# Kernel tuning notes

Measured on AMD Instinct MI355X. Metric: run time of the kernel, lower is better.

The kernel has to match this reference:

```python
import jax, jax.numpy as jnp
import numpy as np

D_MODEL = 1024
NUM_HEADS = 16
HEAD = D_MODEL // NUM_HEADS
SCALE = float(np.sqrt(D_MODEL))  # note: sqrt(d_model), as in source
LN_EPS = 1e-5


def setup_inputs() -> dict:
    key = jax.random.key(0)
    ks = jax.random.split(key, 12)
    B, Sq, Skv = 2, 2048, 2048
    s = 0.02
    return {
        "x": jax.random.normal(ks[0], (B, Sq, D_MODEL), jnp.float32),
        "enc_output": jax.random.normal(ks[1], (B, Skv, D_MODEL), jnp.float32),
        "Wq": jax.random.normal(ks[2], (D_MODEL, D_MODEL), jnp.float32) * s,
        "bq": jnp.zeros((D_MODEL,), jnp.float32),
        "Wk": jax.random.normal(ks[3], (D_MODEL, D_MODEL), jnp.float32) * s,
        "bk": jnp.zeros((D_MODEL,), jnp.float32),
        "Wv": jax.random.normal(ks[4], (D_MODEL, D_MODEL), jnp.float32) * s,
        "bv": jnp.zeros((D_MODEL,), jnp.float32),
        "Wo": jax.random.normal(ks[5], (D_MODEL, D_MODEL), jnp.float32) * s,
        "bo": jnp.zeros((D_MODEL,), jnp.float32),
        "gamma": jnp.ones((D_MODEL,), jnp.float32),
        "beta": jnp.zeros((D_MODEL,), jnp.float32),
    }


def _split_heads(t):
    B, S, _ = t.shape
    return t.reshape(B, S, NUM_HEADS, HEAD).transpose(0, 2, 1, 3)  # [B,H,S,hd]


def reference(x, enc_output, Wq, bq, Wk, bk, Wv, bv, Wo, bo, gamma, beta):
    q = _split_heads(x @ Wq.T + bq)           # [B,H,Sq,hd]
    k = _split_heads(enc_output @ Wk.T + bk)  # [B,H,Skv,hd]
    v = _split_heads(enc_output @ Wv.T + bv)  # [B,H,Skv,hd]
    scores = jnp.einsum("bhqd,bhkd->bhqk", q, k) / SCALE
    attn_weights = jax.nn.softmax(scores, axis=-1)  # dropout p=0 -> identity
    ctx = jnp.einsum("bhqk,bhkd->bhqd", attn_weights, v)
    B, H, Sq, hd = ctx.shape
    ctx = ctx.transpose(0, 2, 1, 3).reshape(B, Sq, H * hd)
    proj = ctx @ Wo.T + bo
    y = x + proj
    mu = jnp.mean(y, axis=-1, keepdims=True)
    var = jnp.var(y, axis=-1, keepdims=True)
    out = (y - mu) * jax.lax.rsqrt(var + LN_EPS) * gamma + beta
    return out, attn_weights
```

## Files before the change

### kernel.cpp

```cpp
#include <hip/hip_runtime.h>

typedef __attribute__((ext_vector_type(4))) float f32x4;
typedef __attribute__((ext_vector_type(8))) short bf16x8;
typedef __attribute__((ext_vector_type(4))) short s16x4;
typedef unsigned short u16;

#define GLOAD_LDS16(g, l)                                                      \
  __builtin_amdgcn_global_load_lds(                                            \
      (__attribute__((address_space(1))) const void*)(g),                      \
      (__attribute__((address_space(3))) void*)(l), 16, 0, 0)

static __device__ __forceinline__ u16 f2b(float f) {
  unsigned u = __builtin_bit_cast(unsigned, f);
  unsigned r = (u + 0x7fffu + ((u >> 16) & 1u)) >> 16;
  return (u16)r;
}

static __device__ __forceinline__ f32x4 mfma16(bf16x8 a, bf16x8 b, f32x4 c) {
  return __builtin_amdgcn_mfma_f32_16x16x32_bf16(a, b, c, 0, 0, 0);
}

static __device__ __forceinline__ int fsw(int row) {
  return (row & 7) ^ ((row & 8) >> 1);
}

__global__ __launch_bounds__(256) void cvt_bf16(const float* __restrict__ in,
                                                u16* __restrict__ out, int n4) {
  int i = blockIdx.x * 256 + threadIdx.x;
  int stride = gridDim.x * 256;
  for (; i < n4; i += stride) {
    float4 v = ((const float4*)in)[i];
    s16x4 o;
    o[0] = (short)f2b(v.x);
    o[1] = (short)f2b(v.y);
    o[2] = (short)f2b(v.z);
    o[3] = (short)f2b(v.w);
    ((s16x4*)out)[i] = o;
  }
}

#define QSCALE 0.0450842200278f
__global__ __launch_bounds__(256) void gemm_qkv3(
    const u16* __restrict__ xb, const u16* __restrict__ eb,
    const u16* __restrict__ Wqb, const u16* __restrict__ Wkb,
    const u16* __restrict__ Wvb, const float* __restrict__ bq,
    const float* __restrict__ bk, const float* __restrict__ bv,
    u16* __restrict__ Qd, u16* __restrict__ Kd, u16* __restrict__ Vtd) {
  __shared__ __align__(16) u16 As[128 * 32];
  __shared__ __align__(16) u16 Bs[128 * 32];
  const int K = 1024;
  int z = blockIdx.z;
  const u16* A = (z == 0) ? xb : eb;
  const u16* W = (z == 0) ? Wqb : (z == 1) ? Wkb : Wvb;
  const float* bias = (z == 0) ? bq : (z == 1) ? bk : bv;

  int tid = threadIdx.x;
  int w = tid >> 6, lane = tid & 63;
  int wr = w >> 1, wc = w & 1;
  int r16 = lane & 15, c4 = lane >> 4;
  int m0 = blockIdx.y * 128, n0 = blockIdx.x * 128;
  int srow = tid >> 2;
  int scol = (tid & 3) * 8;

  f32x4 acc[4][4] = {};

  const u16* ga0 = A + (size_t)(m0 + srow) * K + scol;
  const u16* gb0 = W + (size_t)(n0 + srow) * K + scol;
  char* asb = (char*)As + w * 1024;
  char* bsb = (char*)Bs + w * 1024;

  for (int k0 = 0; k0 < K; k0 += 32) {
    GLOAD_LDS16(ga0 + k0, asb);
    GLOAD_LDS16(ga0 + 64 * K + k0, asb + 4096);
    GLOAD_LDS16(gb0 + k0, bsb);
    GLOAD_LDS16(gb0 + 64 * K + k0, bsb + 4096);
    __syncthreads();
    bf16x8 af[4], bfr[4];
#pragma unroll
    for (int i = 0; i < 4; ++i)
      af[i] = *(const bf16x8*)(As + (wr * 64 + i * 16 + r16) * 32 + c4 * 8);
#pragma unroll
    for (int j = 0; j < 4; ++j)
      bfr[j] = *(const bf16x8*)(Bs + (wc * 64 + j * 16 + r16) * 32 + c4 * 8);
#pragma unroll
    for (int i = 0; i < 4; ++i)
#pragma unroll
      for (int j = 0; j < 4; ++j) acc[i][j] = mfma16(af[i], bfr[j], acc[i][j]);
    __syncthreads();
  }

  if (z < 2) {
    float oscale = (z == 0) ? QSCALE : 1.0f;
    u16* dst = (z == 0) ? Qd : Kd;
#pragma unroll
    for (int i = 0; i < 4; ++i) {
      int m = m0 + wr * 64 + i * 16 + c4 * 4;
      int b = m >> 11, s = m & 2047;
#pragma unroll
      for (int j = 0; j < 4; ++j) {
        int n = n0 + wc * 64 + j * 16 + r16;
        int h = n >> 6, d = n & 63;
        float bv = bias[n];
        u16* dp = dst + (((size_t)(b * 16 + h) * 2048 + s) * 64 + d);
#pragma unroll
        for (int r = 0; r < 4; ++r)
          dp[(size_t)r * 64] = f2b((acc[i][j][r] + bv) * oscale);
      }
    }
  } else {
#pragma unroll
    for (int i = 0; i < 4; ++i) {
      int m = m0 + wr * 64 + i * 16 + c4 * 4;
      int b = m >> 11, s = m & 2047;
#pragma unroll
      for (int j = 0; j < 4; ++j) {
        int n = n0 + wc * 64 + j * 16 + r16;
        int h = n >> 6, d = n & 63;
        float bv = bias[n];
        s16x4 o4;
#pragma unroll
        for (int r = 0; r < 4; ++r) o4[r] = (short)f2b(acc[i][j][r] + bv);
        *(s16x4*)(Vtd + ((size_t)((b * 16 + h) * 64 + d)) * 2048 + s) = o4;
      }
    }
  }
}

__global__ __launch_bounds__(256) void gemm_out(const u16* __restrict__ A,
                                                const u16* __restrict__ W,
                                                const float* __restrict__ bias,
                                                const float* __restrict__ X,
                                                float* __restrict__ Y) {
  __shared__ __align__(16) u16 As[128 * 32];
  __shared__ __align__(16) u16 Bs[128 * 32];
  const int K = 1024;
  int tid = threadIdx.x;
  int w = tid >> 6, lane = tid & 63;
  int wr = w >> 1, wc = w & 1;
  int r16 = lane & 15, c4 = lane >> 4;
  int m0 = blockIdx.y * 128, n0 = blockIdx.x * 128;
  int srow = tid >> 2;
  int scol = (tid & 3) * 8;

  f32x4 acc[4][4] = {};

  const u16* ga0 = A + (size_t)(m0 + srow) * K + scol;
  const u16* gb0 = W + (size_t)(n0 + srow) * K + scol;
  char* asb = (char*)As + w * 1024;
  char* bsb = (char*)Bs + w * 1024;

  for (int k0 = 0; k0 < K; k0 += 32) {
    GLOAD_LDS16(ga0 + k0, asb);
    GLOAD_LDS16(ga0 + 64 * K + k0, asb + 4096);
    GLOAD_LDS16(gb0 + k0, bsb);
    GLOAD_LDS16(gb0 + 64 * K + k0, bsb + 4096);
    __syncthreads();
    bf16x8 af[4], bfr[4];
#pragma unroll
    for (int i = 0; i < 4; ++i)
      af[i] = *(const bf16x8*)(As + (wr * 64 + i * 16 + r16) * 32 + c4 * 8);
#pragma unroll
    for (int j = 0; j < 4; ++j)
      bfr[j] = *(const bf16x8*)(Bs + (wc * 64 + j * 16 + r16) * 32 + c4 * 8);
#pragma unroll
    for (int i = 0; i < 4; ++i)
#pragma unroll
      for (int j = 0; j < 4; ++j) acc[i][j] = mfma16(af[i], bfr[j], acc[i][j]);
    __syncthreads();
  }

#pragma unroll
  for (int i = 0; i < 4; ++i) {
    int m = m0 + wr * 64 + i * 16 + c4 * 4;
#pragma unroll
    for (int j = 0; j < 4; ++j) {
      int n = n0 + wc * 64 + j * 16 + r16;
      float bv = bias[n];
#pragma unroll
      for (int r = 0; r < 4; ++r) {
        size_t idx = (size_t)(m + r) * 1024 + n;
        Y[idx] = acc[i][j][r] + bv + X[idx];
      }
    }
  }
}

__global__ __launch_bounds__(256, 2) void attn_k(const u16* __restrict__ Q,
                                                 const u16* __restrict__ Kg,
                                                 const u16* __restrict__ Vt,
                                                 float* __restrict__ attnw,
                                                 u16* __restrict__ ctx) {
  __shared__ __align__(16) u16 Klds[2][64 * 64];
  __shared__ __align__(16) u16 Vlds[2][64 * 64];

  int tid = threadIdx.x;
  int w = tid >> 6, lane = tid & 63;
  int r16 = lane & 15, c4 = lane >> 4;
  int id = blockIdx.x;
  int bh = id & 31, qt = id >> 5;
  int b = bh >> 4, h = bh & 15;
  int q0 = qt * 128 + w * 32;

  const u16* Qp = Q + ((size_t)bh * 2048 + q0) * 64;
  const u16* Kp = Kg + (size_t)bh * 2048 * 64;
  const u16* Vp = Vt + (size_t)bh * 64 * 2048;

  bf16x8 qf[2][2];
#pragma unroll
  for (int hh = 0; hh < 2; ++hh)
#pragma unroll
    for (int ch = 0; ch < 2; ++ch)
      qf[hh][ch] = *(const bf16x8*)(Qp + (size_t)(hh * 16 + r16) * 64 +
                                    ch * 32 + c4 * 8);

  int perm0 = ((r16 >> 2) << 3) + (r16 & 3);
  int srow0 = w * 8 + (lane >> 3);
  int sc = lane & 7;

#define STAGE_K(bufi, kv)                                                      \
  {                                                                            \
    _Pragma("unroll") for (int i = 0; i < 2; ++i) {                            \
      int row = i * 32 + srow0;                                                \
      int ch = sc ^ fsw(row);                                                  \
      GLOAD_LDS16(Kp + (size_t)((kv) + row) * 64 + ch * 8,                     \
                  (u16*)&Klds[bufi][0] + w * 512 + i * 2048);                  \
    }                                                                          \
  }
#define STAGE_V(bufi, kv)                                                      \
  {                                                                            \
    _Pragma("unroll") for (int i = 0; i < 2; ++i) {                            \
      int row = i * 32 + srow0;                                                \
      int ch = sc ^ fsw(row);                                                  \
      GLOAD_LDS16(Vp + (size_t)row * 2048 + (kv) + ch * 8,                     \
                  (u16*)&Vlds[bufi][0] + w * 512 + i * 2048);                  \
    }                                                                          \
  }
#define LDSF(base, row, chunk)                                                 \
  (*(const bf16x8*)((base) + (row) * 64 + (((chunk) ^ fsw(row)) << 3)))

  float sumA = 0.f, sumB = 0.f;
  STAGE_K(0, 0);
  __syncthreads();
  int buf = 0;
  for (int kv0 = 0; kv0 < 2048; kv0 += 64) {
    if (kv0 + 64 < 2048) STAGE_K(buf ^ 1, kv0 + 64);
    const u16* Kb = &Klds[buf][0];
#pragma unroll
    for (int s = 0; s < 2; ++s) {
      int ra = s * 32 + perm0;
      bf16x8 k00 = LDSF(Kb, ra, c4);
      bf16x8 k01 = LDSF(Kb, ra, c4 + 4);
      bf16x8 k10 = LDSF(Kb, ra + 4, c4);
      bf16x8 k11 = LDSF(Kb, ra + 4, c4 + 4);
      f32x4 s0A = {}, s1A = {}, s0B = {}, s1B = {};
      __builtin_amdgcn_s_setprio(1);
      s0A = mfma16(k00, qf[0][0], s0A);
      s0A = mfma16(k01, qf[0][1], s0A);
      s1A = mfma16(k10, qf[0][0], s1A);
      s1A = mfma16(k11, qf[0][1], s1A);
      s0B = mfma16(k00, qf[1][0], s0B);
      s0B = mfma16(k01, qf[1][1], s0B);
      s1B = mfma16(k10, qf[1][0], s1B);
      s1B = mfma16(k11, qf[1][1], s1B);
      __builtin_amdgcn_s_setprio(0);
#pragma unroll
      for (int r = 0; r < 4; ++r) {
        sumA += __builtin_amdgcn_exp2f(s0A[r]) + __builtin_amdgcn_exp2f(s1A[r]);
        sumB += __builtin_amdgcn_exp2f(s0B[r]) + __builtin_amdgcn_exp2f(s1B[r]);
      }
    }
    __syncthreads();
    buf ^= 1;
  }
  sumA += __shfl_xor(sumA, 16, 64);
  sumA += __shfl_xor(sumA, 32, 64);
  sumB += __shfl_xor(sumB, 16, 64);
  sumB += __shfl_xor(sumB, 32, 64);
  float nlsA = -__log2f(sumA);
  float nlsB = -__log2f(sumB);

  f32x4 oA[4] = {}, oB[4] = {};
  float* apA = attnw + ((size_t)bh * 2048 + q0 + r16) * 2048;
  float* apB = apA + (size_t)16 * 2048;
  STAGE_K(0, 0);
  STAGE_V(0, 0);
  __syncthreads();
  buf = 0;
  for (int kv0 = 0; kv0 < 2048; kv0 += 64) {
    if (kv0 + 64 < 2048) {
      STAGE_K(buf ^ 1, kv0 + 64);
      STAGE_V(buf ^ 1, kv0 + 64);
    }
    const u16* Kb = &Klds[buf][0];
    const u16* Vb = &Vlds[buf][0];
#pragma unroll
    for (int s = 0; s < 2; ++s) {
      int ra = s * 32 + perm0;
      bf16x8 k00 = LDSF(Kb, ra, c4);
      bf16x8 k01 = LDSF(Kb, ra, c4 + 4);
      bf16x8 k10 = LDSF(Kb, ra + 4, c4);
      bf16x8 k11 = LDSF(Kb, ra + 4, c4 + 4);
      f32x4 s0A = {}, s1A = {}, s0B = {}, s1B = {};
      __builtin_amdgcn_s_setprio(1);
      s0A = mfma16(k00, qf[0][0], s0A);
      s0A = mfma16(k01, qf[0][1], s0A);
      s1A = mfma16(k10, qf[0][0], s1A);
      s1A = mfma16(k11, qf[0][1], s1A);
      s0B = mfma16(k00, qf[1][0], s0B);
      s0B = mfma16(k01, qf[1][1], s0B);
      s1B = mfma16(k10, qf[1][0], s1B);
      s1B = mfma16(k11, qf[1][1], s1B);
      __builtin_amdgcn_s_setprio(0);
      f32x4 p0A, p1A, p0B, p1B;
#pragma unroll
      for (int r = 0; r < 4; ++r) {
        p0A[r] = __builtin_amdgcn_exp2f(s0A[r] + nlsA);
        p1A[r] = __builtin_amdgcn_exp2f(s1A[r] + nlsA);
        p0B[r] = __builtin_amdgcn_exp2f(s0B[r] + nlsB);
        p1B[r] = __builtin_amdgcn_exp2f(s1B[r] + nlsB);
      }
      int kvc = kv0 + s * 32 + c4 * 8;
      *(f32x4*)(apA + kvc) = p0A;
      *(f32x4*)(apA + kvc + 4) = p1A;
      *(f32x4*)(apB + kvc) = p0B;
      *(f32x4*)(apB + kvc + 4) = p1B;
      bf16x8 pfA, pfB;
#pragma unroll
      for (int r = 0; r < 4; ++r) {
        pfA[r] = (short)f2b(p0A[r]);
        pfA[r + 4] = (short)f2b(p1A[r]);
        pfB[r] = (short)f2b(p0B[r]);
        pfB[r + 4] = (short)f2b(p1B[r]);
      }
      bf16x8 v0 = LDSF(Vb, 0 * 16 + r16, s * 4 + c4);
      bf16x8 v1 = LDSF(Vb, 1 * 16 + r16, s * 4 + c4);
      bf16x8 v2 = LDSF(Vb, 2 * 16 + r16, s * 4 + c4);
      bf16x8 v3 = LDSF(Vb, 3 * 16 + r16, s * 4 + c4);
      __builtin_amdgcn_s_setprio(1);
      oA[0] = mfma16(pfA, v0, oA[0]);
      oA[1] = mfma16(pfA, v1, oA[1]);
      oA[2] = mfma16(pfA, v2, oA[2]);
      oA[3] = mfma16(pfA, v3, oA[3]);
      oB[0] = mfma16(pfB, v0, oB[0]);
      oB[1] = mfma16(pfB, v1, oB[1]);
      oB[2] = mfma16(pfB, v2, oB[2]);
      oB[3] = mfma16(pfB, v3, oB[3]);
      __builtin_amdgcn_s_setprio(0);
    }
    __syncthreads();
    buf ^= 1;
  }

#pragma unroll
  for (int dt = 0; dt < 4; ++dt)
#pragma unroll
    for (int r = 0; r < 4; ++r) {
      ctx[((size_t)(b * 2048 + q0 + c4 * 4 + r)) * 1024 + h * 64 + dt * 16 +
          r16] = f2b(oA[dt][r]);
      ctx[((size_t)(b * 2048 + q0 + 16 + c4 * 4 + r)) * 1024 + h * 64 +
          dt * 16 + r16] = f2b(oB[dt][r]);
    }
#undef STAGE_K
#undef STAGE_V
#undef LDSF
}

__global__ __launch_bounds__(256) void ln_k(const float* __restrict__ Y,
                                            const float* __restrict__ gamma,
                                            const float* __restrict__ beta,
                                            float* __restrict__ out) {
  int row = blockIdx.x * 4 + (threadIdx.x >> 6);
  int lane = threadIdx.x & 63;
  const float* yr = Y + (size_t)row * 1024;
  float4 v[4];
  float sum = 0.f, sq = 0.f;
#pragma unroll
  for (int i = 0; i < 4; ++i) {
    v[i] = *(const float4*)(yr + i * 256 + lane * 4);
    sum += v[i].x + v[i].y + v[i].z + v[i].w;
    sq += v[i].x * v[i].x + v[i].y * v[i].y + v[i].z * v[i].z + v[i].w * v[i].w;
  }
#pragma unroll
  for (int m = 1; m < 64; m <<= 1) {
    sum += __shfl_xor(sum, m, 64);
    sq += __shfl_xor(sq, m, 64);
  }
  float mu = sum * (1.f / 1024.f);
  float var = sq * (1.f / 1024.f) - mu * mu;
  float rs = rsqrtf(var + 1e-5f);
  float* orow = out + (size_t)row * 1024;
#pragma unroll
  for (int i = 0; i < 4; ++i) {
    int c = i * 256 + lane * 4;
    float4 g = *(const float4*)(gamma + c);
    float4 be = *(const float4*)(beta + c);
    float4 o;
    o.x = (v[i].x - mu) * rs * g.x + be.x;
    o.y = (v[i].y - mu) * rs * g.y + be.y;
    o.z = (v[i].z - mu) * rs * g.z + be.z;
    o.w = (v[i].w - mu) * rs * g.w + be.w;
    *(float4*)(orow + c) = o;
  }
}

extern "C" void kernel_launch(void* const* d_in, const int* in_sizes, int n_in,
                              void* d_out, int out_size, void* d_ws,
                              size_t ws_size, hipStream_t stream) {
  const float* x = (const float*)d_in[0];
  const float* enc = (const float*)d_in[1];
  const float* Wq = (const float*)d_in[2];
  const float* bq = (const float*)d_in[3];
  const float* Wk = (const float*)d_in[4];
  const float* bk = (const float*)d_in[5];
  const float* Wv = (const float*)d_in[6];
  const float* bv = (const float*)d_in[7];
  const float* Wo = (const float*)d_in[8];
  const float* bo = (const float*)d_in[9];
  const float* gamma = (const float*)d_in[10];
  const float* beta = (const float*)d_in[11];

  float* out = (float*)d_out;
  float* attnw = out + (size_t)4194304;

  char* ws = (char*)d_ws;
  u16* xb = (u16*)(ws + (size_t)0);
  u16* eb = (u16*)(ws + ((size_t)8 << 20));
  u16* Wqb = (u16*)(ws + ((size_t)16 << 20));
  u16* Wkb = (u16*)(ws + ((size_t)18 << 20));
  u16* Wvb = (u16*)(ws + ((size_t)20 << 20));
  u16* Wob = (u16*)(ws + ((size_t)22 << 20));
  u16* Qws = (u16*)(ws + ((size_t)24 << 20));
  u16* Kws = (u16*)(ws + ((size_t)32 << 20));
  u16* Vt = (u16*)(ws + ((size_t)48 << 20));
  u16* ctx = (u16*)(ws + ((size_t)40 << 20));
  float* Yws = (float*)(ws + (size_t)0);

  cvt_bf16<<<dim3(1024), 256, 0, stream>>>(x, xb, 1048576);
  cvt_bf16<<<dim3(1024), 256, 0, stream>>>(enc, eb, 1048576);
  cvt_bf16<<<dim3(256), 256, 0, stream>>>(Wq, Wqb, 262144);
  cvt_bf16<<<dim3(256), 256, 0, stream>>>(Wk, Wkb, 262144);
  cvt_bf16<<<dim3(256), 256, 0, stream>>>(Wv, Wvb, 262144);
  cvt_bf16<<<dim3(256), 256, 0, stream>>>(Wo, Wob, 262144);

  gemm_qkv3<<<dim3(8, 32, 3), 256, 0, stream>>>(xb, eb, Wqb, Wkb, Wvb, bq, bk,
                                                bv, Qws, Kws, Vt);

  attn_k<<<dim3(512), 256, 0, stream>>>(Qws, Kws, Vt, attnw, ctx);

  gemm_out<<<dim3(8, 32), 256, 0, stream>>>(ctx, Wob, bo, x, Yws);

  ln_k<<<dim3(1024), 256, 0, stream>>>(Yws, gamma, beta, out);
}
```

Before: 310.8 us.

## Halve attention query tile per wave, double grid, use packed bf16 convert

Each attention wave now handles 16 query rows instead of 32, the grid doubles to 1024 blocks, and launch bounds ask for 4 blocks per CU to raise occupancy. The manual bf16 rounding of probabilities is replaced with the hardware v_cvt_pk_bf16_f32 packed convert. In exchange, K/V tiles staged in LDS are reused across half as many query rows, which doubles K/V LDS staging traffic per output and adds more synchronisation per unit of work.

```diff
diff --git a/kernel.cpp b/kernel.cpp
--- a/kernel.cpp
+++ b/kernel.cpp
@@ -3,6 +3,7 @@
 typedef __attribute__((ext_vector_type(4))) float f32x4;
 typedef __attribute__((ext_vector_type(8))) short bf16x8;
 typedef __attribute__((ext_vector_type(4))) short s16x4;
+typedef __attribute__((ext_vector_type(4))) unsigned u32x4;
 typedef unsigned short u16;
 
 #define GLOAD_LDS16(g, l)                                                      \
@@ -14,6 +15,12 @@
   unsigned u = __builtin_bit_cast(unsigned, f);
   unsigned r = (u + 0x7fffu + ((u >> 16) & 1u)) >> 16;
   return (u16)r;
+}
+
+static __device__ __forceinline__ unsigned pk2(float lo, float hi) {
+  unsigned r;
+  asm("v_cvt_pk_bf16_f32 %0, %1, %2" : "=v"(r) : "v"(lo), "v"(hi));
+  return r;
 }
 
 static __device__ __forceinline__ f32x4 mfma16(bf16x8 a, bf16x8 b, f32x4 c) {
@@ -185,7 +192,7 @@
   }
 }
 
-__global__ __launch_bounds__(256, 2) void attn_k(const u16* __restrict__ Q,
+__global__ __launch_bounds__(256, 4) void attn_k(const u16* __restrict__ Q,
                                                  const u16* __restrict__ Kg,
                                                  const u16* __restrict__ Vt,
                                                  float* __restrict__ attnw,
@@ -199,19 +206,14 @@
   int id = blockIdx.x;
   int bh = id & 31, qt = id >> 5;
   int b = bh >> 4, h = bh & 15;
-  int q0 = qt * 128 + w * 32;
+  int q0 = qt * 64 + w * 16;
 
   const u16* Qp = Q + ((size_t)bh * 2048 + q0) * 64;
   const u16* Kp = Kg + (size_t)bh * 2048 * 64;
   const u16* Vp = Vt + (size_t)bh * 64 * 2048;
 
-  bf16x8 qf[2][2];
-#pragma unroll
-  for (int hh = 0; hh < 2; ++hh)
-#pragma unroll
-    for (int ch = 0; ch < 2; ++ch)
-      qf[hh][ch] = *(const bf16x8*)(Qp + (size_t)(hh * 16 + r16) * 64 +
-                                    ch * 32 + c4 * 8);
+  bf16x8 qf0 = *(const bf16x8*)(Qp + (size_t)r16 * 64 + c4 * 8);
+  bf16x8 qf1 = *(const bf16x8*)(Qp + (size_t)r16 * 64 + 32 + c4 * 8);
 
   int perm0 = ((r16 >> 2) << 3) + (r16 & 3);
   int srow0 = w * 8 + (lane >> 3);
@@ -238,7 +240,7 @@
 #define LDSF(base, row, chunk)                                                 \
   (*(const bf16x8*)((base) + (row) * 64 + (((chunk) ^ fsw(row)) << 3)))
 
-  float sumA = 0.f, sumB = 0.f;
+  float sum = 0.f;
   STAGE_K(0, 0);
   __syncthreads();
   int buf = 0;
@@ -252,36 +254,26 @@
       bf16x8 k01 = LDSF(Kb, ra, c4 + 4);
       bf16x8 k10 = LDSF(Kb, ra + 4, c4);
       bf16x8 k11 = LDSF(Kb, ra + 4, c4 + 4);
-      f32x4 s0A = {}, s1A = {}, s0B = {}, s1B = {};
+      f32x4 s0 = {}, s1 = {};
       __builtin_amdgcn_s_setprio(1);
-      s0A = mfma16(k00, qf[0][0], s0A);
-      s0A = mfma16(k01, qf[0][1], s0A);
-      s1A = mfma16(k10, qf[0][0], s1A);
-      s1A = mfma16(k11, qf[0][1], s1A);
-      s0B = mfma16(k00, qf[1][0], s0B);
-      s0B = mfma16(k01, qf[1][1], s0B);
-      s1B = mfma16(k10, qf[1][0], s1B);
-      s1B = mfma16(k11, qf[1][1], s1B);
+      s0 = mfma16(k00, qf0, s0);
+      s0 = mfma16(k01, qf1, s0);
+      s1 = mfma16(k10, qf0, s1);
+      s1 = mfma16(k11, qf1, s1);
       __builtin_amdgcn_s_setprio(0);
 #pragma unroll
-      for (int r = 0; r < 4; ++r) {
-        sumA += __builtin_amdgcn_exp2f(s0A[r]) + __builtin_amdgcn_exp2f(s1A[r]);
-        sumB += __builtin_amdgcn_exp2f(s0B[r]) + __builtin_amdgcn_exp2f(s1B[r]);
-      }
+      for (int r = 0; r < 4; ++r)
+        sum += __builtin_amdgcn_exp2f(s0[r]) + __builtin_amdgcn_exp2f(s1[r]);
     }
     __syncthreads();
     buf ^= 1;
   }
-  sumA += __shfl_xor(sumA, 16, 64);
-  sumA += __shfl_xor(sumA, 32, 64);
-  sumB += __shfl_xor(sumB, 16, 64);
-  sumB += __shfl_xor(sumB, 32, 64);
-  float nlsA = -__log2f(sumA);
-  float nlsB = -__log2f(sumB);
-
-  f32x4 oA[4] = {}, oB[4] = {};
-  float* apA = attnw + ((size_t)bh * 2048 + q0 + r16) * 2048;
-  float* apB = apA + (size_t)16 * 2048;
+  sum += __shfl_xor(sum, 16, 64);
+  sum += __shfl_xor(sum, 32, 64);
+  float nls = -__log2f(sum);
+
+  f32x4 o[4] = {};
+  float* ap = attnw + ((size_t)bh * 2048 + q0 + r16) * 2048;
   STAGE_K(0, 0);
   STAGE_V(0, 0);
   __syncthreads();
@@ -300,51 +292,37 @@
       bf16x8 k01 = LDSF(Kb, ra, c4 + 4);
       bf16x8 k10 = LDSF(Kb, ra + 4, c4);
       bf16x8 k11 = LDSF(Kb, ra + 4, c4 + 4);
-      f32x4 s0A = {}, s1A = {}, s0B = {}, s1B = {};
+      f32x4 s0 = {}, s1 = {};
       __builtin_amdgcn_s_setprio(1);
-      s0A = mfma16(k00, qf[0][0], s0A);
-      s0A = mfma16(k01, qf[0][1], s0A);
-      s1A = mfma16(k10, qf[0][0], s1A);
-      s1A = mfma16(k11, qf[0][1], s1A);
-      s0B = mfma16(k00, qf[1][0], s0B);
-      s0B = mfma16(k01, qf[1][1], s0B);
-      s1B = mfma16(k10, qf[1][0], s1B);
-      s1B = mfma16(k11, qf[1][1], s1B);
+      s0 = mfma16(k00, qf0, s0);
+      s0 = mfma16(k01, qf1, s0);
+      s1 = mfma16(k10, qf0, s1);
+      s1 = mfma16(k11, qf1, s1);
       __builtin_amdgcn_s_setprio(0);
-      f32x4 p0A, p1A, p0B, p1B;
+      f32x4 p0, p1;
 #pragma unroll
       for (int r = 0; r < 4; ++r) {
-        p0A[r] = __builtin_amdgcn_exp2f(s0A[r] + nlsA);
-        p1A[r] = __builtin_amdgcn_exp2f(s1A[r] + nlsA);
-        p0B[r] = __builtin_amdgcn_exp2f(s0B[r] + nlsB);
-        p1B[r] = __builtin_amdgcn_exp2f(s1B[r] + nlsB);
+        p0[r] = __builtin_amdgcn_exp2f(s0[r] + nls);
+        p1[r] = __builtin_amdgcn_exp2f(s1[r] + nls);
       }
       int kvc = kv0 + s * 32 + c4 * 8;
-      *(f32x4*)(apA + kvc) = p0A;
-      *(f32x4*)(apA + kvc + 4) = p1A;
-      *(f32x4*)(apB + kvc) = p0B;
-      *(f32x4*)(apB + kvc + 4) = p1B;
-      bf16x8 pfA, pfB;
-#pragma unroll
-      for (int r = 0; r < 4; ++r) {
-        pfA[r] = (short)f2b(p0A[r]);
-        pfA[r + 4] = (short)f2b(p1A[r]);
-        pfB[r] = (short)f2b(p0B[r]);
-        pfB[r + 4] = (short)f2b(p1B[r]);
-      }
+      *(f32x4*)(ap + kvc) = p0;
+      *(f32x4*)(ap + kvc + 4) = p1;
+      u32x4 pk;
+      pk[0] = pk2(p0[0], p0[1]);
+      pk[1] = pk2(p0[2], p0[3]);
+      pk[2] = pk2(p1[0], p1[1]);
+      pk[3] = pk2(p1[2], p1[3]);
+      bf16x8 pf = __builtin_bit_cast(bf16x8, pk);
       bf16x8 v0 = LDSF(Vb, 0 * 16 + r16, s * 4 + c4);
       bf16x8 v1 = LDSF(Vb, 1 * 16 + r16, s * 4 + c4);
       bf16x8 v2 = LDSF(Vb, 2 * 16 + r16, s * 4 + c4);
       bf16x8 v3 = LDSF(Vb, 3 * 16 + r16, s * 4 + c4);
       __builtin_amdgcn_s_setprio(1);
-      oA[0] = mfma16(pfA, v0, oA[0]);
-      oA[1] = mfma16(pfA, v1, oA[1]);
-      oA[2] = mfma16(pfA, v2, oA[2]);
-      oA[3] = mfma16(pfA, v3, oA[3]);
-      oB[0] = mfma16(pfB, v0, oB[0]);
-      oB[1] = mfma16(pfB, v1, oB[1]);
-      oB[2] = mfma16(pfB, v2, oB[2]);
-      oB[3] = mfma16(pfB, v3, oB[3]);
+      o[0] = mfma16(pf, v0, o[0]);
+      o[1] = mfma16(pf, v1, o[1]);
+      o[2] = mfma16(pf, v2, o[2]);
+      o[3] = mfma16(pf, v3, o[3]);
       __builtin_amdgcn_s_setprio(0);
     }
     __syncthreads();
@@ -354,12 +332,9 @@
 #pragma unroll
   for (int dt = 0; dt < 4; ++dt)
 #pragma unroll
-    for (int r = 0; r < 4; ++r) {
+    for (int r = 0; r < 4; ++r)
       ctx[((size_t)(b * 2048 + q0 + c4 * 4 + r)) * 1024 + h * 64 + dt * 16 +
-          r16] = f2b(oA[dt][r]);
-      ctx[((size_t)(b * 2048 + q0 + 16 + c4 * 4 + r)) * 1024 + h * 64 +
-          dt * 16 + r16] = f2b(oB[dt][r]);
-    }
+          r16] = f2b(o[dt][r]);
 #undef STAGE_K
 #undef STAGE_V
 #undef LDSF
@@ -445,7 +420,7 @@
   gemm_qkv3<<<dim3(8, 32, 3), 256, 0, stream>>>(xb, eb, Wqb, Wkb, Wvb, bq, bk,
                                                 bv, Qws, Kws, Vt);
 
-  attn_k<<<dim3(512), 256, 0, stream>>>(Qws, Kws, Vt, attnw, ctx);
+  attn_k<<<dim3(1024), 256, 0, stream>>>(Qws, Kws, Vt, attnw, ctx);
 
   gemm_out<<<dim3(8, 32), 256, 0, stream>>>(ctx, Wob, bo, x, Yws);
 
```

Result: faster. 304.3 us (-2.1%).
